# Performance work log

Hardware: AMD Instinct MI355X
Metric: run time of the kernel (lower is better)

## Reference

```python
import jax, jax.numpy as jnp
import numpy as np

N_EXPERTS = 64
TOPK = 4
DIM = 2048
B_T = 8192


def setup_inputs() -> dict:
    key = jax.random.key(0)
    k1, k2 = jax.random.split(key)
    x = jax.random.normal(k1, (B_T, DIM), jnp.float32)
    W = jax.random.normal(k2, (N_EXPERTS, DIM), jnp.float32) * 0.02  # nn.Linear weight (out, in)
    router_bias = jnp.zeros((N_EXPERTS,), jnp.float32)  # registered buffer, init zeros
    return {"x": x, "W": W, "router_bias": router_bias, "token_capacity": 3072}


def _route(x, W, router_bias, token_capacity):
    """Faithful serial greedy capacity-aware routing.

    Replicates the torch nested loop (k-major, token-minor order):
      - per step, pick argmax over the token's (mutated) logits among experts
        with remaining capacity;
      - full experts whose logit exceeds the chosen one get permanently set
        to -inf in that token's logit row (exactly what the inner while-style
        loop does);
      - if no expert has capacity, selected stays -1, weight 0, and the whole
        row becomes -inf (torch sets the top expert to -inf n_experts times).
    """
    logits0 = x @ W.T + router_bias                       # (N, E)
    scores = jax.nn.softmax(logits0, axis=-1)             # (N, E)
    cap = token_capacity // TOPK                          # python int
    remaining0 = jnp.full((N_EXPERTS,), float(cap), jnp.float32)
    N = x.shape[0]
    NEG = jnp.float32(-jnp.inf)

    def step(carry, i):
        logits, remaining = carry
        b = i % N                                         # token index (k-major order)
        row = logits[b]                                   # (E,)
        masked = jnp.where(remaining > 0, row, NEG)
        chosen = jnp.argmax(masked)
        ok = remaining[chosen] > 0                        # False only if all experts full
        sel = jnp.where(ok, chosen, -1).astype(jnp.int32)
        w = jnp.where(ok, scores[b, chosen], jnp.float32(0.0))
        full = remaining <= 0
        cval = row[chosen]
        # full experts 'above' the chosen one were visited and zapped to -inf
        new_row = jnp.where(ok,
                            jnp.where(full & (row > cval), NEG, row),
                            jnp.full_like(row, NEG))
        logits = logits.at[b].set(new_row)
        remaining = remaining.at[chosen].add(jnp.where(ok, jnp.float32(-1.0), jnp.float32(0.0)))
        return (logits, remaining), (sel, w)

    (_, _), (sel_f, w_f) = jax.lax.scan(step, (logits0, remaining0),
                                        jnp.arange(TOPK * N))
    selected = sel_f.reshape(TOPK, N).T                   # (N, TOPK)
    weights = w_f.reshape(TOPK, N).T                      # (N, TOPK)
    weights = weights / (weights.sum(axis=-1, keepdims=True) + 1e-8)
    return selected, weights


def reference(x, W, router_bias, token_capacity):
    return _route(x, W, router_bias, token_capacity)
```

## Files before the change

### kernel.cpp

```cpp
#include <hip/hip_runtime.h>
#include <math.h>

#define N_TOK 8192
#define DIM   2048
#define NE    64
#define TOPK  4
#define THETA 2e-3f
#define TPB2  16
#define NBLK  (N_TOK / TPB2)
#define RSTR  260

typedef short bf16x8 __attribute__((ext_vector_type(8)));
typedef float f32x4  __attribute__((ext_vector_type(4)));

#define OFF_LOGITS 0
#define OFF_MAXV   (OFF_LOGITS + N_TOK * NE)
#define OFF_DENOM  (OFF_MAXV + N_TOK)
#define OFF_W1     (OFF_DENOM + N_TOK)
#define OFF_C1     (OFF_W1 + N_TOK)
#define OFF_NFLAG  (OFF_C1 + N_TOK)
#define OFF_FLAGL  (OFF_NFLAG + 64)
#define OFF_WH     (OFF_FLAGL + N_TOK)
#define OFF_WL     (OFF_WH + NE * DIM / 2)
#define OFF_WT     (OFF_WL + NE * DIM / 2)
#define OFF_WTMP   (OFF_WT + NE * DIM)

__device__ inline void cvt2(float a, float b, unsigned& hi, unsigned& lo) {
    const unsigned ua = __float_as_uint(a), ub = __float_as_uint(b);
    hi = __builtin_amdgcn_perm(ub, ua, 0x07060302u);
    const float ra = a - __uint_as_float(ua & 0xFFFF0000u);
    const float rb = b - __uint_as_float(ub & 0xFFFF0000u);
    lo = __builtin_amdgcn_perm(__float_as_uint(rb), __float_as_uint(ra), 0x07060302u);
}

union FragU { unsigned u[4]; bf16x8 v; uint4 q; };

__device__ inline void make_frags(const float4& p, const float4& q,
                                  bf16x8& hi, bf16x8& lo) {
    FragU H, L;
    cvt2(p.x, p.y, H.u[0], L.u[0]);
    cvt2(p.z, p.w, H.u[1], L.u[1]);
    cvt2(q.x, q.y, H.u[2], L.u[2]);
    cvt2(q.z, q.w, H.u[3], L.u[3]);
    hi = H.v; lo = L.v;
}

__global__ __launch_bounds__(256)
void k_wc(const float* __restrict__ W, unsigned short* __restrict__ wh2,
          unsigned short* __restrict__ wl2, float* __restrict__ wt,
          int* __restrict__ nflag) {
    const int t = blockIdx.x * 256 + threadIdx.x;
    if (t == 0) nflag[0] = 0;
    const int l  = t & 63;
    const int grp = t >> 6;
    const int nt = grp & 3;
    const int kc = grp >> 2;
    const int e  = nt * 16 + (l & 15);
    const int k0 = kc * 32 + (l >> 4) * 8;

    const float4 p = *reinterpret_cast<const float4*>(W + (size_t)e * DIM + k0);
    const float4 q = *reinterpret_cast<const float4*>(W + (size_t)e * DIM + k0 + 4);
    FragU H, L;
    cvt2(p.x, p.y, H.u[0], L.u[0]);
    cvt2(p.z, p.w, H.u[1], L.u[1]);
    cvt2(q.x, q.y, H.u[2], L.u[2]);
    cvt2(q.z, q.w, H.u[3], L.u[3]);
    const size_t off = (size_t)grp * 512 + l * 8;
    *reinterpret_cast<uint4*>(wh2 + off) = H.q;
    *reinterpret_cast<uint4*>(wl2 + off) = L.q;

    wt[(size_t)(k0 + 0) * NE + e] = p.x;
    wt[(size_t)(k0 + 1) * NE + e] = p.y;
    wt[(size_t)(k0 + 2) * NE + e] = p.z;
    wt[(size_t)(k0 + 3) * NE + e] = p.w;
    wt[(size_t)(k0 + 4) * NE + e] = q.x;
    wt[(size_t)(k0 + 5) * NE + e] = q.y;
    wt[(size_t)(k0 + 6) * NE + e] = q.z;
    wt[(size_t)(k0 + 7) * NE + e] = q.w;
}

__global__ __launch_bounds__(512, 4)
void k_main(const float* __restrict__ x, const unsigned short* __restrict__ wh2,
            const unsigned short* __restrict__ wl2, const float* __restrict__ bias,
            float* __restrict__ logits, float* __restrict__ maxv,
            float* __restrict__ denomv, float* __restrict__ w1f,
            int* __restrict__ c1, int* __restrict__ nflag, int* __restrict__ flagl) {
    __shared__ __align__(16) float xs[2][TPB2 * RSTR];
    __shared__ float red[8][TPB2][68];
    __shared__ float lbuf[TPB2][68];

    const int tid = threadIdx.x;
    const int w   = tid >> 6;
    const int l   = tid & 63;
    const int t0  = blockIdx.x * TPB2;
    const int m   = l & 15;
    const int g   = l >> 4;

    const float* xrow0 = x + (size_t)(t0 + 2 * w) * DIM + l * 4;
    const float* xrow1 = x + (size_t)(t0 + 2 * w + 1) * DIM + l * 4;
    float* st0 = &xs[0][(2 * w) * RSTR + l * 4];
    float* st1 = &xs[0][(2 * w + 1) * RSTR + l * 4];
    const int xs1off = TPB2 * RSTR;

    const unsigned short* bh = wh2 + (size_t)w * 2048 + l * 8;
    const unsigned short* bl = wl2 + (size_t)w * 2048 + l * 8;

    f32x4 accA[4], accB[4];
    #pragma unroll
    for (int nt = 0; nt < 4; ++nt)
        #pragma unroll
        for (int r = 0; r < 4; ++r) { accA[nt][r] = 0.0f; accB[nt][r] = 0.0f; }

    {
        const float4 r0 = *reinterpret_cast<const float4*>(xrow0);
        const float4 r1 = *reinterpret_cast<const float4*>(xrow1);
        *reinterpret_cast<float4*>(st0) = r0;
        *reinterpret_cast<float4*>(st1) = r1;
    }
    uint4 BH[2][4], BL[2][4];
    #pragma unroll
    for (int nt = 0; nt < 4; ++nt) {
        BH[0][nt] = *reinterpret_cast<const uint4*>(bh + nt * 512);
        BL[0][nt] = *reinterpret_cast<const uint4*>(bl + nt * 512);
    }
    __syncthreads();

    const int aoff = m * RSTR + w * 32 + g * 8;

    #pragma unroll
    for (int win = 0; win < 8; ++win) {
        const int cur = win & 1, nxt = cur ^ 1;
        float4 nx0, nx1;
        if (win < 7) {
            nx0 = *reinterpret_cast<const float4*>(xrow0 + (win + 1) * 256);
            nx1 = *reinterpret_cast<const float4*>(xrow1 + (win + 1) * 256);
            #pragma unroll
            for (int nt = 0; nt < 4; ++nt) {
                BH[nxt][nt] = *reinterpret_cast<const uint4*>(
                    bh + (size_t)(win + 1) * 16384 + nt * 512);
                BL[nxt][nt] = *reinterpret_cast<const uint4*>(
                    bl + (size_t)(win + 1) * 16384 + nt * 512);
            }
        }

        const float4 p = *reinterpret_cast<const float4*>(&xs[0][cur * xs1off + aoff]);
        const float4 q = *reinterpret_cast<const float4*>(&xs[0][cur * xs1off + aoff + 4]);
        bf16x8 ah, al;
        make_frags(p, q, ah, al);

        #pragma unroll
        for (int nt = 0; nt < 4; ++nt) {
            FragU b; b.q = BH[cur][nt];
            accA[nt] = __builtin_amdgcn_mfma_f32_16x16x32_bf16(ah, b.v, accA[nt], 0, 0, 0);
            accB[nt] = __builtin_amdgcn_mfma_f32_16x16x32_bf16(al, b.v, accB[nt], 0, 0, 0);
        }
        #pragma unroll
        for (int nt = 0; nt < 4; ++nt) {
            FragU b; b.q = BL[cur][nt];
            accB[nt] = __builtin_amdgcn_mfma_f32_16x16x32_bf16(ah, b.v, accB[nt], 0, 0, 0);
        }

        if (win < 7) {
            *reinterpret_cast<float4*>(st0 + nxt * xs1off) = nx0;
            *reinterpret_cast<float4*>(st1 + nxt * xs1off) = nx1;
        }
        __syncthreads();
    }

    #pragma unroll
    for (int nt = 0; nt < 4; ++nt)
        #pragma unroll
        for (int r = 0; r < 4; ++r)
            red[w][g * 4 + r][nt * 16 + m] = accA[nt][r] + accB[nt][r];
    __syncthreads();

    for (int e2 = tid; e2 < TPB2 * NE; e2 += 512) {
        const int t = e2 >> 6, e = e2 & 63;
        float s = red[0][t][e];
        #pragma unroll
        for (int ww = 1; ww < 8; ++ww) s += red[ww][t][e];
        s += bias[e];
        logits[(size_t)(t0 + t) * NE + e] = s;
        lbuf[t][e] = s;
    }
    __syncthreads();

    #pragma unroll
    for (int tt = 0; tt < 2; ++tt) {
        const int t = w * 2 + tt;
        const float lv = lbuf[t][l];
        float v1 = lv; int i1 = l; float v2 = -INFINITY;
        #pragma unroll
        for (int off = 32; off; off >>= 1) {
            const float ov1 = __shfl_xor(v1, off);
            const int   oi1 = __shfl_xor(i1, off);
            const float ov2 = __shfl_xor(v2, off);
            if (ov1 > v1 || (ov1 == v1 && oi1 < i1)) {
                v2 = fmaxf(v1, ov2); v1 = ov1; i1 = oi1;
            } else {
                v2 = fmaxf(v2, ov1);
            }
        }
        float s = expf(lv - v1);
        #pragma unroll
        for (int off = 32; off; off >>= 1) s += __shfl_xor(s, off);
        if (l == 0) {
            const int row = t0 + t;
            maxv[row]   = v1;
            denomv[row] = s;
            c1[row]     = i1;
            w1f[row]    = 1.0f / s;
            if (v1 - v2 < THETA) {
                const int ix = atomicAdd(nflag, 1);
                flagl[ix] = row;
            }
        }
    }
}

__global__ __launch_bounds__(256)
void k_exact(const int* __restrict__ nflag, const int* __restrict__ flagl,
             const float* __restrict__ x, const float* __restrict__ wt,
             const float* __restrict__ bias, float* __restrict__ logits,
             float* __restrict__ maxv, float* __restrict__ denomv,
             float* __restrict__ w1f, int* __restrict__ c1) {
    __shared__ float part[4][68];
    const int n   = nflag[0];
    const int tid = threadIdx.x;
    const int w   = tid >> 6, l = tid & 63;
    for (int i = blockIdx.x; i < n; i += 64) {
        const int t = flagl[i];
        const float* xr = x + (size_t)t * DIM + w * 512;
        const float* wb = wt + (size_t)(w * 512) * NE + l;
        float a = 0.0f;
        for (int k = 0; k < 512; k += 4) {
            const float4 xv = *reinterpret_cast<const float4*>(xr + k);
            a = fmaf(xv.x, wb[(size_t)(k + 0) * NE], a);
            a = fmaf(xv.y, wb[(size_t)(k + 1) * NE], a);
            a = fmaf(xv.z, wb[(size_t)(k + 2) * NE], a);
            a = fmaf(xv.w, wb[(size_t)(k + 3) * NE], a);
        }
        part[w][l] = a;
        __syncthreads();
        if (w == 0) {
            float lg = bias[l];
            #pragma unroll
            for (int s = 0; s < 4; ++s) lg += part[s][l];
            logits[(size_t)t * NE + l] = lg;
            float v = lg; int idx = l;
            #pragma unroll
            for (int off = 32; off; off >>= 1) {
                const float ov = __shfl_xor(v, off);
                const int   oi = __shfl_xor(idx, off);
                if (ov > v || (ov == v && oi < idx)) { v = ov; idx = oi; }
            }
            float p = expf(lg - v);
            #pragma unroll
            for (int off = 32; off; off >>= 1) p += __shfl_xor(p, off);
            if (l == 0) {
                maxv[t]   = v;
                denomv[t] = p;
                c1[t]     = idx;
                w1f[t]    = 1.0f / p;
            }
        }
        __syncthreads();
    }
}

__global__ __launch_bounds__(256)
void k_decide(const int* __restrict__ c1, const float* __restrict__ w1,
              const float* __restrict__ logits, const float* __restrict__ maxv,
              const float* __restrict__ denomv, const int* __restrict__ tc,
              float* __restrict__ out, float* __restrict__ wtmp) {
    __shared__ int hist[NE];
    __shared__ int flagS;
    const int tid = threadIdx.x;
    if (tid < NE) hist[tid] = 0;
    __syncthreads();
    for (int i = tid; i < N_TOK; i += 256) atomicAdd(&hist[c1[i]], 1);
    __syncthreads();
    const int cap = tc[0] / TOPK;
    if (tid < NE) {
        const bool bad = (TOPK * hist[tid] > cap);
        const unsigned long long mm = __ballot(bad);
        if (tid == 0) flagS = (mm == 0ull) ? 1 : 0;
    }
    __syncthreads();

    if (flagS) {
        const int b = blockIdx.x * 256 + tid;
        const float se = (float)c1[b];
        const float wv = w1[b];
        const float wn = wv / (4.0f * wv + 1e-8f);
        *reinterpret_cast<float4*>(out + (size_t)b * 4) = make_float4(se, se, se, se);
        *reinterpret_cast<float4*>(out + (size_t)N_TOK * TOPK + (size_t)b * 4) =
            make_float4(wn, wn, wn, wn);
        return;
    }

    if (blockIdx.x != 0) return;
    if (tid < 64) {
        const int e = tid;
        int rem = cap;
        for (int k = 0; k < TOPK; ++k) {
            for (int b = 0; b < N_TOK; ++b) {
                const float lg = logits[(size_t)b * NE + e];
                float v = (rem > 0) ? lg : -INFINITY;
                int idx = e;
                #pragma unroll
                for (int off = 32; off; off >>= 1) {
                    const float ov = __shfl_xor(v, off);
                    const int   oi = __shfl_xor(idx, off);
                    if (ov > v || (ov == v && oi < idx)) { v = ov; idx = oi; }
                }
                const bool ok = (v != -INFINITY);
                if (ok && e == idx) rem -= 1;
                const float lc = __shfl(lg, idx);
                if (e == 0) {
                    out[(size_t)b * TOPK + k]  = ok ? (float)idx : -1.0f;
                    wtmp[(size_t)b * TOPK + k] = ok ? expf(lc - maxv[b]) / denomv[b] : 0.0f;
                }
            }
        }
    }
    __syncthreads();
    for (int b = tid; b < N_TOK; b += 256) {
        const float w0 = wtmp[b * 4 + 0], w1_ = wtmp[b * 4 + 1];
        const float w2 = wtmp[b * 4 + 2], w3 = wtmp[b * 4 + 3];
        const float s = ((w0 + w1_) + w2) + w3 + 1e-8f;
        out[N_TOK * TOPK + b * 4 + 0] = w0 / s;
        out[N_TOK * TOPK + b * 4 + 1] = w1_ / s;
        out[N_TOK * TOPK + b * 4 + 2] = w2 / s;
        out[N_TOK * TOPK + b * 4 + 3] = w3 / s;
    }
}

extern "C" void kernel_launch(void* const* d_in, const int* in_sizes, int n_in,
                              void* d_out, int out_size, void* d_ws, size_t ws_size,
                              hipStream_t stream) {
    const float* x    = (const float*)d_in[0];
    const float* W    = (const float*)d_in[1];
    const float* bias = (const float*)d_in[2];
    const int*   tc   = (const int*)d_in[3];

    float* ws       = (float*)d_ws;
    float* logits   = ws + OFF_LOGITS;
    float* maxv     = ws + OFF_MAXV;
    float* denomv   = ws + OFF_DENOM;
    float* w1f      = ws + OFF_W1;
    int*   c1       = (int*)(ws + OFF_C1);
    int*   nflag    = (int*)(ws + OFF_NFLAG);
    int*   flagl    = (int*)(ws + OFF_FLAGL);
    unsigned short* wh2 = (unsigned short*)(ws + OFF_WH);
    unsigned short* wl2 = (unsigned short*)(ws + OFF_WL);
    float* wt       = ws + OFF_WT;
    float* wtmp     = ws + OFF_WTMP;
    float* out      = (float*)d_out;

    k_wc<<<NE * DIM / 8 / 256, 256, 0, stream>>>(W, wh2, wl2, wt, nflag);
    k_main<<<NBLK, 512, 0, stream>>>(x, wh2, wl2, bias, logits, maxv, denomv,
                                     w1f, c1, nflag, flagl);
    k_exact<<<64, 256, 0, stream>>>(nflag, flagl, x, wt, bias, logits,
                                    maxv, denomv, w1f, c1);
    k_decide<<<N_TOK / 256, 256, 0, stream>>>(c1, w1f, logits, maxv, denomv,
                                              tc, out, wtmp);
}
```

Measured before the change: 131.8 us.

## Process 32 tokens per block with 16 waves and global expert histogram

The main GEMM kernel now handles 32 tokens per 1024-thread block. It uses 16 waves that split K into 16 chunks and reuse each weight fragment for two 16-row M tiles, which halves weight traffic per token. The x staging switches from double-buffered to single-buffered with register prefetch, and a two-stage cross-wave reduction is added. The top-1 expert histogram is now built with global atomics in k_main (corrected in k_exact) instead of every k_decide block recounting 8192 tokens. Risks include lower occupancy from the larger LDS and block size, extra syncs, and global atomic contention.

```diff
diff --git a/kernel.cpp b/kernel.cpp
--- a/kernel.cpp
+++ b/kernel.cpp
@@ -6,9 +6,9 @@
 #define NE    64
 #define TOPK  4
 #define THETA 2e-3f
-#define TPB2  16
+#define TPB2  32
 #define NBLK  (N_TOK / TPB2)
-#define RSTR  260
+#define RSTR  516
 
 typedef short bf16x8 __attribute__((ext_vector_type(8)));
 typedef float f32x4  __attribute__((ext_vector_type(4)));
@@ -19,7 +19,8 @@
 #define OFF_W1     (OFF_DENOM + N_TOK)
 #define OFF_C1     (OFF_W1 + N_TOK)
 #define OFF_NFLAG  (OFF_C1 + N_TOK)
-#define OFF_FLAGL  (OFF_NFLAG + 64)
+#define OFF_GHIST  (OFF_NFLAG + 64)
+#define OFF_FLAGL  (OFF_GHIST + 64)
 #define OFF_WH     (OFF_FLAGL + N_TOK)
 #define OFF_WL     (OFF_WH + NE * DIM / 2)
 #define OFF_WT     (OFF_WL + NE * DIM / 2)
@@ -48,9 +49,10 @@
 __global__ __launch_bounds__(256)
 void k_wc(const float* __restrict__ W, unsigned short* __restrict__ wh2,
           unsigned short* __restrict__ wl2, float* __restrict__ wt,
-          int* __restrict__ nflag) {
+          int* __restrict__ nflag, int* __restrict__ ghist) {
     const int t = blockIdx.x * 256 + threadIdx.x;
-    if (t == 0) nflag[0] = 0;
+    if (t < NE) ghist[t] = 0;
+    if (t == NE) nflag[0] = 0;
     const int l  = t & 63;
     const int grp = t >> 6;
     const int nt = grp & 3;
@@ -79,13 +81,14 @@
     wt[(size_t)(k0 + 7) * NE + e] = q.w;
 }
 
-__global__ __launch_bounds__(512, 4)
+__global__ __launch_bounds__(1024, 4)
 void k_main(const float* __restrict__ x, const unsigned short* __restrict__ wh2,
             const unsigned short* __restrict__ wl2, const float* __restrict__ bias,
             float* __restrict__ logits, float* __restrict__ maxv,
             float* __restrict__ denomv, float* __restrict__ w1f,
-            int* __restrict__ c1, int* __restrict__ nflag, int* __restrict__ flagl) {
-    __shared__ __align__(16) float xs[2][TPB2 * RSTR];
+            int* __restrict__ c1, int* __restrict__ nflag, int* __restrict__ flagl,
+            int* __restrict__ ghist) {
+    __shared__ __align__(16) float xs[TPB2 * RSTR];
     __shared__ float red[8][TPB2][68];
     __shared__ float lbuf[TPB2][68];
 
@@ -96,92 +99,119 @@
     const int m   = l & 15;
     const int g   = l >> 4;
 
-    const float* xrow0 = x + (size_t)(t0 + 2 * w) * DIM + l * 4;
-    const float* xrow1 = x + (size_t)(t0 + 2 * w + 1) * DIM + l * 4;
-    float* st0 = &xs[0][(2 * w) * RSTR + l * 4];
-    float* st1 = &xs[0][(2 * w + 1) * RSTR + l * 4];
-    const int xs1off = TPB2 * RSTR;
+    const int srow = tid >> 5;
+    const int sc   = tid & 31;
+    const float* xsrc = x + (size_t)(t0 + srow) * DIM + sc * 4;
+    float* sdst = &xs[srow * RSTR + sc * 4];
 
     const unsigned short* bh = wh2 + (size_t)w * 2048 + l * 8;
     const unsigned short* bl = wl2 + (size_t)w * 2048 + l * 8;
 
-    f32x4 accA[4], accB[4];
+    f32x4 acc[2][4];
     #pragma unroll
-    for (int nt = 0; nt < 4; ++nt)
-        #pragma unroll
-        for (int r = 0; r < 4; ++r) { accA[nt][r] = 0.0f; accB[nt][r] = 0.0f; }
+    for (int mt = 0; mt < 2; ++mt)
+        #pragma unroll
+        for (int nt = 0; nt < 4; ++nt)
+            #pragma unroll
+            for (int r = 0; r < 4; ++r) acc[mt][nt][r] = 0.0f;
+
+    float4 pf[4];
+    #pragma unroll
+    for (int j = 0; j < 4; ++j)
+        pf[j] = *reinterpret_cast<const float4*>(xsrc + j * 128);
+    #pragma unroll
+    for (int j = 0; j < 4; ++j)
+        *reinterpret_cast<float4*>(sdst + j * 128) = pf[j];
+    __syncthreads();
+
+    const int aoff = m * RSTR + w * 32 + g * 8;
+
+    #pragma unroll
+    for (int win = 0; win < 4; ++win) {
+        if (win < 3) {
+            #pragma unroll
+            for (int j = 0; j < 4; ++j)
+                pf[j] = *reinterpret_cast<const float4*>(
+                    xsrc + (size_t)(win + 1) * 512 + j * 128);
+        }
+        uint4 BH[4], BL[4];
+        #pragma unroll
+        for (int nt = 0; nt < 4; ++nt) {
+            BH[nt] = *reinterpret_cast<const uint4*>(bh + (size_t)win * 32768 + nt * 512);
+            BL[nt] = *reinterpret_cast<const uint4*>(bl + (size_t)win * 32768 + nt * 512);
+        }
+        const float4 p0 = *reinterpret_cast<const float4*>(&xs[aoff]);
+        const float4 q0 = *reinterpret_cast<const float4*>(&xs[aoff + 4]);
+        const float4 p1 = *reinterpret_cast<const float4*>(&xs[aoff + 16 * RSTR]);
+        const float4 q1 = *reinterpret_cast<const float4*>(&xs[aoff + 16 * RSTR + 4]);
+        bf16x8 ah0, al0, ah1, al1;
+        make_frags(p0, q0, ah0, al0);
+        make_frags(p1, q1, ah1, al1);
+
+        #pragma unroll
+        for (int nt = 0; nt < 4; ++nt) {
+            FragU b; b.q = BH[nt];
+            acc[0][nt] = __builtin_amdgcn_mfma_f32_16x16x32_bf16(ah0, b.v, acc[0][nt], 0, 0, 0);
+            acc[1][nt] = __builtin_amdgcn_mfma_f32_16x16x32_bf16(ah1, b.v, acc[1][nt], 0, 0, 0);
+            acc[0][nt] = __builtin_amdgcn_mfma_f32_16x16x32_bf16(al0, b.v, acc[0][nt], 0, 0, 0);
+            acc[1][nt] = __builtin_amdgcn_mfma_f32_16x16x32_bf16(al1, b.v, acc[1][nt], 0, 0, 0);
+        }
+        #pragma unroll
+        for (int nt = 0; nt < 4; ++nt) {
+            FragU b; b.q = BL[nt];
+            acc[0][nt] = __builtin_amdgcn_mfma_f32_16x16x32_bf16(ah0, b.v, acc[0][nt], 0, 0, 0);
+            acc[1][nt] = __builtin_amdgcn_mfma_f32_16x16x32_bf16(ah1, b.v, acc[1][nt], 0, 0, 0);
+        }
+        __syncthreads();
+        if (win < 3) {
+            #pragma unroll
+            for (int j = 0; j < 4; ++j)
+                *reinterpret_cast<float4*>(sdst + j * 128) = pf[j];
+            __syncthreads();
+        }
+    }
+
+    if (w >= 8) {
+        #pragma unroll
+        for (int mt = 0; mt < 2; ++mt)
+            #pragma unroll
+            for (int nt = 0; nt < 4; ++nt)
+                #pragma unroll
+                for (int r = 0; r < 4; ++r)
+                    red[w - 8][mt * 16 + g * 4 + r][nt * 16 + m] = acc[mt][nt][r];
+    }
+    __syncthreads();
+    if (w < 8) {
+        #pragma unroll
+        for (int mt = 0; mt < 2; ++mt)
+            #pragma unroll
+            for (int nt = 0; nt < 4; ++nt)
+                #pragma unroll
+                for (int r = 0; r < 4; ++r)
+                    acc[mt][nt][r] += red[w][mt * 16 + g * 4 + r][nt * 16 + m];
+    }
+    __syncthreads();
+    if (w < 8) {
+        #pragma unroll
+        for (int mt = 0; mt < 2; ++mt)
+            #pragma unroll
+            for (int nt = 0; nt < 4; ++nt)
+                #pragma unroll
+                for (int r = 0; r < 4; ++r)
+                    red[w][mt * 16 + g * 4 + r][nt * 16 + m] = acc[mt][nt][r];
+    }
+    __syncthreads();
 
     {
-        const float4 r0 = *reinterpret_cast<const float4*>(xrow0);
-        const float4 r1 = *reinterpret_cast<const float4*>(xrow1);
-        *reinterpret_cast<float4*>(st0) = r0;
-        *reinterpret_cast<float4*>(st1) = r1;
-    }
-    uint4 BH[2][4], BL[2][4];
-    #pragma unroll
-    for (int nt = 0; nt < 4; ++nt) {
-        BH[0][nt] = *reinterpret_cast<const uint4*>(bh + nt * 512);
-        BL[0][nt] = *reinterpret_cast<const uint4*>(bl + nt * 512);
-    }
-    __syncthreads();
-
-    const int aoff = m * RSTR + w * 32 + g * 8;
-
-    #pragma unroll
-    for (int win = 0; win < 8; ++win) {
-        const int cur = win & 1, nxt = cur ^ 1;
-        float4 nx0, nx1;
-        if (win < 7) {
-            nx0 = *reinterpret_cast<const float4*>(xrow0 + (win + 1) * 256);
-            nx1 = *reinterpret_cast<const float4*>(xrow1 + (win + 1) * 256);
-            #pragma unroll
-            for (int nt = 0; nt < 4; ++nt) {
-                BH[nxt][nt] = *reinterpret_cast<const uint4*>(
-                    bh + (size_t)(win + 1) * 16384 + nt * 512);
-                BL[nxt][nt] = *reinterpret_cast<const uint4*>(
-                    bl + (size_t)(win + 1) * 16384 + nt * 512);
-            }
-        }
-
-        const float4 p = *reinterpret_cast<const float4*>(&xs[0][cur * xs1off + aoff]);
-        const float4 q = *reinterpret_cast<const float4*>(&xs[0][cur * xs1off + aoff + 4]);
-        bf16x8 ah, al;
-        make_frags(p, q, ah, al);
-
-        #pragma unroll
-        for (int nt = 0; nt < 4; ++nt) {
-            FragU b; b.q = BH[cur][nt];
-            accA[nt] = __builtin_amdgcn_mfma_f32_16x16x32_bf16(ah, b.v, accA[nt], 0, 0, 0);
-            accB[nt] = __builtin_amdgcn_mfma_f32_16x16x32_bf16(al, b.v, accB[nt], 0, 0, 0);
-        }
-        #pragma unroll
-        for (int nt = 0; nt < 4; ++nt) {
-            FragU b; b.q = BL[cur][nt];
-            accB[nt] = __builtin_amdgcn_mfma_f32_16x16x32_bf16(ah, b.v, accB[nt], 0, 0, 0);
-        }
-
-        if (win < 7) {
-            *reinterpret_cast<float4*>(st0 + nxt * xs1off) = nx0;
-            *reinterpret_cast<float4*>(st1 + nxt * xs1off) = nx1;
-        }
-        __syncthreads();
-    }
-
-    #pragma unroll
-    for (int nt = 0; nt < 4; ++nt)
-        #pragma unroll
-        for (int r = 0; r < 4; ++r)
-            red[w][g * 4 + r][nt * 16 + m] = accA[nt][r] + accB[nt][r];
-    __syncthreads();
-
-    for (int e2 = tid; e2 < TPB2 * NE; e2 += 512) {
-        const int t = e2 >> 6, e = e2 & 63;
-        float s = red[0][t][e];
-        #pragma unroll
-        for (int ww = 1; ww < 8; ++ww) s += red[ww][t][e];
-        s += bias[e];
-        logits[(size_t)(t0 + t) * NE + e] = s;
-        lbuf[t][e] = s;
+        const int t = (tid * 2) >> 6;
+        const int e = (tid * 2) & 63;
+        float s0 = red[0][t][e], s1 = red[0][t][e + 1];
+        #pragma unroll
+        for (int s = 1; s < 8; ++s) { s0 += red[s][t][e]; s1 += red[s][t][e + 1]; }
+        s0 += bias[e]; s1 += bias[e + 1];
+        *reinterpret_cast<float2*>(&logits[(size_t)(t0 + t) * NE + e]) =
+            make_float2(s0, s1);
+        lbuf[t][e] = s0; lbuf[t][e + 1] = s1;
     }
     __syncthreads();
 
@@ -210,6 +240,7 @@
             denomv[row] = s;
             c1[row]     = i1;
             w1f[row]    = 1.0f / s;
+            atomicAdd(&ghist[i1], 1);
             if (v1 - v2 < THETA) {
                 const int ix = atomicAdd(nflag, 1);
                 flagl[ix] = row;
@@ -223,7 +254,8 @@
              const float* __restrict__ x, const float* __restrict__ wt,
              const float* __restrict__ bias, float* __restrict__ logits,
              float* __restrict__ maxv, float* __restrict__ denomv,
-             float* __restrict__ w1f, int* __restrict__ c1) {
+             float* __restrict__ w1f, int* __restrict__ c1,
+             int* __restrict__ ghist) {
     __shared__ float part[4][68];
     const int n   = nflag[0];
     const int tid = threadIdx.x;
@@ -258,10 +290,15 @@
             #pragma unroll
             for (int off = 32; off; off >>= 1) p += __shfl_xor(p, off);
             if (l == 0) {
+                const int old = c1[t];
                 maxv[t]   = v;
                 denomv[t] = p;
                 c1[t]     = idx;
                 w1f[t]    = 1.0f / p;
+                if (idx != old) {
+                    atomicAdd(&ghist[old], -1);
+                    atomicAdd(&ghist[idx], 1);
+                }
             }
         }
         __syncthreads();
@@ -272,17 +309,13 @@
 void k_decide(const int* __restrict__ c1, const float* __restrict__ w1,
               const float* __restrict__ logits, const float* __restrict__ maxv,
               const float* __restrict__ denomv, const int* __restrict__ tc,
-              float* __restrict__ out, float* __restrict__ wtmp) {
-    __shared__ int hist[NE];
+              const int* __restrict__ ghist, float* __restrict__ out,
+              float* __restrict__ wtmp) {
     __shared__ int flagS;
     const int tid = threadIdx.x;
-    if (tid < NE) hist[tid] = 0;
-    __syncthreads();
-    for (int i = tid; i < N_TOK; i += 256) atomicAdd(&hist[c1[i]], 1);
-    __syncthreads();
     const int cap = tc[0] / TOPK;
     if (tid < NE) {
-        const bool bad = (TOPK * hist[tid] > cap);
+        const bool bad = (TOPK * ghist[tid] > cap);
         const unsigned long long mm = __ballot(bad);
         if (tid == 0) flagS = (mm == 0ull) ? 1 : 0;
     }
@@ -351,6 +384,7 @@
     float* w1f      = ws + OFF_W1;
     int*   c1       = (int*)(ws + OFF_C1);
     int*   nflag    = (int*)(ws + OFF_NFLAG);
+    int*   ghist    = (int*)(ws + OFF_GHIST);
     int*   flagl    = (int*)(ws + OFF_FLAGL);
     unsigned short* wh2 = (unsigned short*)(ws + OFF_WH);
     unsigned short* wl2 = (unsigned short*)(ws + OFF_WL);
@@ -358,11 +392,11 @@
     float* wtmp     = ws + OFF_WTMP;
     float* out      = (float*)d_out;
 
-    k_wc<<<NE * DIM / 8 / 256, 256, 0, stream>>>(W, wh2, wl2, wt, nflag);
-    k_main<<<NBLK, 512, 0, stream>>>(x, wh2, wl2, bias, logits, maxv, denomv,
-                                     w1f, c1, nflag, flagl);
+    k_wc<<<NE * DIM / 8 / 256, 256, 0, stream>>>(W, wh2, wl2, wt, nflag, ghist);
+    k_main<<<NBLK, 1024, 0, stream>>>(x, wh2, wl2, bias, logits, maxv, denomv,
+                                      w1f, c1, nflag, flagl, ghist);
     k_exact<<<64, 256, 0, stream>>>(nflag, flagl, x, wt, bias, logits,
-                                    maxv, denomv, w1f, c1);
+                                    maxv, denomv, w1f, c1, ghist);
     k_decide<<<N_TOK / 256, 256, 0, stream>>>(c1, w1f, logits, maxv, denomv,
-                                              tc, out, wtmp);
-}
+                                              tc, ghist, out, wtmp);
+}
```

Result: slower. 177.6 us (+34.8%).
